# Kernel optimization log

Measured on AMD Instinct MI355X. Metric: run time of the kernel, lower is better.

Reference implementation:

```python
import jax, jax.numpy as jnp
import numpy as np

B, S = 2, 2048
HID = 2560
NH, NKV, HD = 20, 5, 128
GROUPS = NH // NKV  # 4
THETA = 500000.0
RMS_EPS = 1e-6  # RMSNorm default eps used for attn_sub_norm
NEG_INF = -1e9


def pack_ternary(key, M, K):
    """Pack ternary weights {-1,0,1} (stored as trits {0,1,2}) into SIMD
    block-interleaved uint8 layout: per 128-elem block, byte j holds
    weights j+0 (bits 6:7), j+32 (4:5), j+64 (2:3), j+96 (0:1)."""
    t = jax.random.randint(key, (M, K), 0, 3).astype(jnp.uint8)
    t = t.reshape(M, K // 128, 4, 32)
    byte = (t[:, :, 0] << 6) | (t[:, :, 1] << 4) | (t[:, :, 2] << 2) | t[:, :, 3]
    return byte.reshape(M, K // 4)


def unpack_ternary(packed):
    """Inverse of pack_ternary -> float weights in {-1,0,1}. (M, K//4) -> (M, K)."""
    M, Kp = packed.shape
    nb = Kp // 32
    b = packed.reshape(M, nb, 32)
    fields = jnp.stack([(b >> 6) & 3, (b >> 4) & 3, (b >> 2) & 3, b & 3], axis=2)
    return fields.reshape(M, nb * 128).astype(jnp.float32) - 1.0


def bitlinear(x, packed, scale):
    w = unpack_ternary(packed) * scale  # (out, in)
    return jnp.einsum('bsi,oi->bso', x, w)


def rotate_half(x):
    h = x.shape[-1] // 2
    return jnp.concatenate([-x[..., h:], x[..., :h]], axis=-1)


def rms_norm(x, w, eps=RMS_EPS):
    var = jnp.mean(jnp.square(x.astype(jnp.float32)), axis=-1, keepdims=True)
    return (w * (x * jax.lax.rsqrt(var + eps))).astype(x.dtype)


def setup_inputs() -> dict:
    key = jax.random.key(0)
    ks = jax.random.split(key, 6)
    hidden_states = jax.random.normal(ks[0], (B, S, HID), dtype=jnp.float32)
    causal = jnp.tril(jnp.ones((S, S), dtype=bool))
    attention_mask = jnp.where(causal, 0.0, NEG_INF).astype(jnp.float32)[None, None]
    return {
        'hidden_states': hidden_states,
        'attention_mask': attention_mask,
        'q_w': pack_ternary(ks[1], NH * HD, HID),
        'k_w': pack_ternary(ks[2], NKV * HD, HID),
        'v_w': pack_ternary(ks[3], NKV * HD, HID),
        'o_w': pack_ternary(ks[4], HID, NH * HD),
        'q_scale': jnp.float32(0.02),
        'k_scale': jnp.float32(0.02),
        'v_scale': jnp.float32(0.02),
        'o_scale': jnp.float32(0.02),
        'attn_norm_w': jnp.ones((NH * HD,), dtype=jnp.float32),
    }


def reference(hidden_states, attention_mask, q_w, k_w, v_w, o_w,
              q_scale, k_scale, v_scale, o_scale, attn_norm_w):
    bsz, seq_len, _ = hidden_states.shape
    q = bitlinear(hidden_states, q_w, q_scale)
    k = bitlinear(hidden_states, k_w, k_scale)
    v = bitlinear(hidden_states, v_w, v_scale)
    q = q.reshape(bsz, seq_len, NH, HD).transpose(0, 2, 1, 3)    # (b,h,s,d)
    k = k.reshape(bsz, seq_len, NKV, HD).transpose(0, 2, 1, 3)
    v = v.reshape(bsz, seq_len, NKV, HD).transpose(0, 2, 1, 3)
    # rotary embedding
    inv_freq = 1.0 / (THETA ** (jnp.arange(0, HD, 2, dtype=jnp.float32) / HD))
    t = jnp.arange(seq_len, dtype=jnp.float32)
    freqs = t[:, None] * inv_freq[None, :]            # (s, d/2)
    emb = jnp.concatenate([freqs, freqs], axis=-1)    # (s, d)
    cos, sin = jnp.cos(emb), jnp.sin(emb)
    q = q * cos + rotate_half(q) * sin
    k = k * cos + rotate_half(k) * sin
    # GQA: repeat kv heads
    k = jnp.repeat(k, GROUPS, axis=1)
    v = jnp.repeat(v, GROUPS, axis=1)
    scores = jnp.einsum('bhqd,bhkd->bhqk', q, k) / np.sqrt(HD).astype(np.float32)
    scores = scores + attention_mask
    attn = jax.nn.softmax(scores.astype(jnp.float32), axis=-1).astype(q.dtype)
    out = jnp.einsum('bhqk,bhkd->bhqd', attn, v)
    out = out.transpose(0, 2, 1, 3).reshape(bsz, seq_len, NH * HD)
    out = rms_norm(out, attn_norm_w)
    return bitlinear(out, o_w, o_scale)
```

## Files before the change

kernel.cpp:

```cpp
#include <hip/hip_runtime.h>
#include <cstdint>
#include <cstddef>

typedef __bf16 bf16x8 __attribute__((ext_vector_type(8)));
typedef float  f32x4  __attribute__((ext_vector_type(4)));
typedef int    i32x4  __attribute__((ext_vector_type(4)));
typedef unsigned short u16x4 __attribute__((ext_vector_type(4)));

#define DEV __device__ __forceinline__
#define NEGINF (-__builtin_inff())

DEV uint16_t f2bf(float f) {
  union { float f; uint32_t u; } v; v.f = f;
  uint32_t u = v.u;
  u += 0x7FFFu + ((u >> 16) & 1u);
  return (uint16_t)(u >> 16);
}
DEV float bf2f(uint16_t h) {
  union { uint32_t u; float f; } v; v.u = ((uint32_t)h) << 16;
  return v.f;
}

DEV void gload_lds16(const void* g, void* l) {
  __builtin_amdgcn_global_load_lds(
      (const __attribute__((address_space(1))) void*)g,
      (__attribute__((address_space(3))) void*)l, 16, 0, 0);
}


__global__ void k_f32_to_bf16(const float* __restrict__ in, uint16_t* __restrict__ out, int n4) {
  int i = blockIdx.x * blockDim.x + threadIdx.x;
  if (i >= n4) return;
  f32x4 v = *(const f32x4*)(in + (size_t)i * 4);
  u16x4 o;
  o[0] = f2bf(v[0]); o[1] = f2bf(v[1]); o[2] = f2bf(v[2]); o[3] = f2bf(v[3]);
  *(u16x4*)(out + (size_t)i * 4) = o;
}

__global__ void k_unpack_all(const uint32_t* __restrict__ qw, const uint32_t* __restrict__ kw,
                             const uint32_t* __restrict__ vw, const uint32_t* __restrict__ ow,
                             uint16_t* __restrict__ wqkv, uint16_t* __restrict__ owb,
                             const float* __restrict__ g) {
  int idx = blockIdx.x * blockDim.x + threadIdx.x;
  if (idx >= 4096000) return;
  if (idx < 2457600) {
    int local = (idx < 1638400) ? idx : ((idx < 2048000) ? idx - 1638400 : idx - 2048000);
    const uint32_t* s = (idx < 1638400) ? qw : ((idx < 2048000) ? kw : vw);
    uint32_t b = s[local] & 0xFFu;
    int drow = idx / 640, pc = idx - drow * 640;
    int blk = pc >> 5, j = pc & 31;
    size_t base = (size_t)drow * 2560 + (size_t)blk * 128 + j;
    wqkv[base]      = f2bf((float)((b >> 6) & 3u) - 1.0f);
    wqkv[base + 32] = f2bf((float)((b >> 4) & 3u) - 1.0f);
    wqkv[base + 64] = f2bf((float)((b >> 2) & 3u) - 1.0f);
    wqkv[base + 96] = f2bf((float)(b & 3u) - 1.0f);
  } else {
    int local = idx - 2457600;
    uint32_t b = ow[local] & 0xFFu;
    int drow = local / 640, pc = local - drow * 640;
    int blk = pc >> 5, j = pc & 31;
    int kpos = blk * 128 + j;
    size_t base = (size_t)drow * 2560 + kpos;
    owb[base]      = f2bf(((float)((b >> 6) & 3u) - 1.0f) * g[kpos]);
    owb[base + 32] = f2bf(((float)((b >> 4) & 3u) - 1.0f) * g[kpos + 32]);
    owb[base + 64] = f2bf(((float)((b >> 2) & 3u) - 1.0f) * g[kpos + 64]);
    owb[base + 96] = f2bf(((float)(b & 3u) - 1.0f) * g[kpos + 96]);
  }
}

__global__ void k_rope_table(float* __restrict__ cosT, float* __restrict__ sinT) {
  int idx = blockIdx.x * blockDim.x + threadIdx.x;
  int s = idx >> 6, i = idx & 63;
  float inv = expf((float)i * (-13.122363377404328f / 64.0f));
  float fr = (float)s * inv;
  cosT[idx] = cosf(fr);
  sinT[idx] = sinf(fr);
}

__global__ void k_rope(uint16_t* __restrict__ buf, const float* __restrict__ cosT,
                       const float* __restrict__ sinT, int H, int total) {
  int idx = blockIdx.x * blockDim.x + threadIdx.x;
  if (idx >= total) return;
  int d = idx & 63;
  int t = idx >> 6;
  int h = t % H;
  int row = t / H;
  int s = row & 2047;
  size_t base = (size_t)row * (size_t)(H * 128) + (size_t)h * 128 + d;
  float x1 = bf2f(buf[base]), x2 = bf2f(buf[base + 64]);
  float c = cosT[(s << 6) + d], sn = sinT[(s << 6) + d];
  buf[base]      = f2bf(x1 * c - x2 * sn);
  buf[base + 64] = f2bf(x2 * c + x1 * sn);
}

template<int MODE>
__global__ __launch_bounds__(256, 2)
void k_gemm(const uint16_t* __restrict__ A, const uint16_t* __restrict__ W,
            uint16_t* __restrict__ Qo, uint16_t* __restrict__ Ko, uint16_t* __restrict__ Vo,
            float* __restrict__ Fo,
            const float* __restrict__ s0p, const float* __restrict__ s1p, const float* __restrict__ s2p,
            int M, int N, int K)
{
  __shared__ uint16_t As[128 * 64];
  __shared__ uint16_t Bs[128 * 64];
  const int tid = threadIdx.x;
  const int n0 = blockIdx.x * 128, m0 = blockIdx.y * 128;
  const int lane = tid & 63, w = tid >> 6;
  const int wm = (w >> 1) * 64, wn = (w & 1) * 64;
  const int lr = lane & 15, lg = lane >> 4, lk = lg * 8;
  const size_t K2 = (size_t)K * 2;
  f32x4 acc[4][4] = {};

  const int srow = tid >> 3;
  const int cprime = ((tid & 7) * 16) ^ ((srow & 7) << 4);
  const uint8_t* Ag = (const uint8_t*)A + (size_t)(m0 + srow) * K2 + cprime;
  const uint8_t* Wg = (const uint8_t*)W + (size_t)(n0 + srow) * K2 + cprime;
  char* Al = (char*)As + w * 1024;
  char* Bl = (char*)Bs + w * 1024;

  for (size_t k0b = 0; k0b < K2; k0b += 128) {
    #pragma unroll
    for (int i = 0; i < 4; ++i)
      gload_lds16(Ag + (size_t)(i * 32) * K2 + k0b, Al + i * 4096);
    #pragma unroll
    for (int i = 0; i < 4; ++i)
      gload_lds16(Wg + (size_t)(i * 32) * K2 + k0b, Bl + i * 4096);
    __syncthreads();
    #pragma unroll
    for (int kc = 0; kc < 64; kc += 32) {
      bf16x8 a[4], b[4];
      #pragma unroll
      for (int i = 0; i < 4; ++i) {
        const int r = wm + i * 16 + lr;
        a[i] = *(const bf16x8*)((const char*)As + r * 128 + (((kc + lk) * 2) ^ ((r & 7) << 4)));
      }
      #pragma unroll
      for (int j = 0; j < 4; ++j) {
        const int r = wn + j * 16 + lr;
        b[j] = *(const bf16x8*)((const char*)Bs + r * 128 + (((kc + lk) * 2) ^ ((r & 7) << 4)));
      }
      #pragma unroll
      for (int i = 0; i < 4; ++i)
        #pragma unroll
        for (int j = 0; j < 4; ++j)
          acc[i][j] = __builtin_amdgcn_mfma_f32_16x16x32_bf16(a[i], b[j], acc[i][j], 0, 0, 0);
    }
    __syncthreads();
  }

  if (MODE == 0) {
    const float qs = *s0p, ks = *s1p, vs = *s2p;
    #pragma unroll
    for (int i = 0; i < 4; ++i) {
      const int rowb = m0 + wm + i * 16 + lg * 4;
      #pragma unroll
      for (int j = 0; j < 4; ++j) {
        const int col = n0 + wn + j * 16 + lr;
        #pragma unroll
        for (int r = 0; r < 4; ++r) {
          const int rr = rowb + r;
          const float v = acc[i][j][r];
          if (col < 2560) {
            Qo[(size_t)rr * 2560 + col] = f2bf(v * qs);
          } else if (col < 3200) {
            Ko[(size_t)rr * 640 + (col - 2560)] = f2bf(v * ks);
          } else {
            const int n2 = col - 3200;
            const int kvh = n2 >> 7, d = n2 & 127;
            const int bb = rr >> 11, ss = rr & 2047;
            Vo[(((size_t)(bb * 5 + kvh) * 128 + d) << 11) + ss] = f2bf(v * vs);
          }
        }
      }
    }
  } else {
    const float os = *s0p;
    #pragma unroll
    for (int i = 0; i < 4; ++i) {
      const int rowb = m0 + wm + i * 16 + lg * 4;
      #pragma unroll
      for (int j = 0; j < 4; ++j) {
        const int col = n0 + wn + j * 16 + lr;
        #pragma unroll
        for (int r = 0; r < 4; ++r)
          Fo[(size_t)(rowb + r) * N + col] = acc[i][j][r] * os * s1p[rowb + r];
      }
    }
  }
}

__global__ __launch_bounds__(256, 2)
void k_attn(const uint16_t* __restrict__ Q, const uint16_t* __restrict__ Kb,
            const uint16_t* __restrict__ Vt, uint16_t* __restrict__ Ob,
            const float* __restrict__ cosT, const float* __restrict__ sinT)
{
  __shared__ char Klds[2][16384];
  __shared__ char Vlds[2][16384];
  __shared__ uint16_t p_lds[4][16][72];

  const int lin = blockIdx.x;
  const int gslot = (lin & 7) * 80 + (lin >> 3);
  const int bk = gslot >> 6;
  const int st = 63 - (gslot & 63);
  const int b = bk / 5, kvh = bk - b * 5;

  const int tid = threadIdx.x, lane = tid & 63, w = tid >> 6;
  const int lr = lane & 15, lg = lane >> 4, lk = lg * 8;
  const int h = kvh * 4 + w;
  uint16_t (*pl)[72] = p_lds[w];
  const int kswz = (lr & 7) << 4;

  const uint8_t* Kg = (const uint8_t*)(Kb + (size_t)b * 2048 * 640 + (size_t)kvh * 128);
  const uint8_t* Vg = (const uint8_t*)(Vt + ((size_t)(b * 5 + kvh) * 128) * 2048);

  const int krow = tid >> 4;
  const int kcol = ((tid & 15) * 16) ^ ((krow & 7) << 4);
  const int vrow = tid >> 3;
  const int vcol = ((tid & 7) * 16) ^ ((vrow & 7) << 4);
  const int dst16 = tid * 16;

  const float C = 0.127531019577f;

  const int q0 = st * 32;
  const int ns = (q0 + 95) >> 6;

  bf16x8 qf0[4], qf1[4];
  {
    const size_t qb0 = ((size_t)(b * 2048 + q0 + lr)) * 2560 + (size_t)h * 128 + lk;
    #pragma unroll
    for (int c = 0; c < 4; ++c) {
      qf0[c] = *(const bf16x8*)&Q[qb0 + c * 32];
      qf1[c] = *(const bf16x8*)&Q[qb0 + 16 * 2560 + c * 32];
    }
  }
  #pragma unroll
  for (int g = 0; g < 2; ++g) {
    bf16x8* qf = g ? qf1 : qf0;
    const int s = q0 + 16 * g + lr;
    const int tb0 = s * 64 + lg * 8;
    #pragma unroll
    for (int c = 0; c < 2; ++c) {
      const int tb = tb0 + c * 32;
      f32x4 csa = *(const f32x4*)&cosT[tb];
      f32x4 csb = *(const f32x4*)&cosT[tb + 4];
      f32x4 sna = *(const f32x4*)&sinT[tb];
      f32x4 snb = *(const f32x4*)&sinT[tb + 4];
      #pragma unroll
      for (int j = 0; j < 8; ++j) {
        const float cs = (j < 4) ? csa[j] : csb[j - 4];
        const float sn = (j < 4) ? sna[j] : snb[j - 4];
        const float x1 = (float)qf[c][j], x2 = (float)qf[c + 2][j];
        qf[c][j]     = (__bf16)(x1 * cs - x2 * sn);
        qf[c + 2][j] = (__bf16)(x2 * cs + x1 * sn);
      }
    }
  }

  {
    const uint8_t* Ks = Kg + (size_t)krow * 1280 + kcol;
    const uint8_t* Vs = Vg + (size_t)vrow * 4096 + vcol;
    #pragma unroll
    for (int i = 0; i < 4; ++i) gload_lds16(Ks + (size_t)i * 16 * 1280, Klds[0] + dst16 + i * 4096);
    #pragma unroll
    for (int i = 0; i < 4; ++i) gload_lds16(Vs + (size_t)i * 32 * 4096, Vlds[0] + dst16 + i * 4096);
  }

  int cur = 0;
  float m0 = NEGINF, m1 = NEGINF, l0 = 0.f, l1 = 0.f;
  f32x4 oa0[8] = {}, oa1[8] = {};

  #pragma unroll 1
  for (int stp = 0; stp < ns; ++stp) {
    const int k0 = stp * 64;
    __syncthreads();

    if (stp + 1 < ns) {
      const int kn = k0 + 64;
      const uint8_t* Ks = Kg + (size_t)(kn + krow) * 1280 + kcol;
      const uint8_t* Vs = Vg + (size_t)vrow * 4096 + (size_t)kn * 2 + vcol;
      char* Kd = Klds[cur ^ 1] + dst16;
      char* Vd = Vlds[cur ^ 1] + dst16;
      #pragma unroll
      for (int i = 0; i < 4; ++i) gload_lds16(Ks + (size_t)i * 16 * 1280, Kd + i * 4096);
      #pragma unroll
      for (int i = 0; i < 4; ++i) gload_lds16(Vs + (size_t)i * 32 * 4096, Vd + i * 4096);
    }

    const char* Kc = Klds[cur];
    const char* Vc = Vlds[cur];

    __builtin_amdgcn_s_setprio(1);
    f32x4 sa0[4] = {}, sa1[4] = {};
    #pragma unroll
    for (int t = 0; t < 4; ++t) {
      #pragma unroll
      for (int c = 0; c < 4; ++c) {
        bf16x8 kf = *(const bf16x8*)(Kc + (t * 16 + lr) * 256 + ((c * 64 + lg * 16) ^ kswz));
        sa0[t] = __builtin_amdgcn_mfma_f32_16x16x32_bf16(kf, qf0[c], sa0[t], 0, 0, 0);
        sa1[t] = __builtin_amdgcn_mfma_f32_16x16x32_bf16(kf, qf1[c], sa1[t], 0, 0, 0);
      }
    }
    __builtin_amdgcn_s_setprio(0);

    #pragma unroll
    for (int g = 0; g < 2; ++g) {
      const f32x4* sa = g ? sa1 : sa0;
      f32x4* oa = g ? oa1 : oa0;
      float& m = g ? m1 : m0;
      float& l = g ? l1 : l0;
      const int q0g = q0 + 16 * g;

      float sraw[16];
      if (k0 + 63 > q0g) {
        #pragma unroll
        for (int t = 0; t < 4; ++t)
          #pragma unroll
          for (int r = 0; r < 4; ++r)
            sraw[t * 4 + r] = (k0 + t * 16 + lg * 4 + r <= q0g + lr) ? sa[t][r] : NEGINF;
      } else {
        #pragma unroll
        for (int t = 0; t < 4; ++t)
          #pragma unroll
          for (int r = 0; r < 4; ++r)
            sraw[t * 4 + r] = sa[t][r];
      }
      float a01 = fmaxf(sraw[0], sraw[1]),   a23 = fmaxf(sraw[2], sraw[3]);
      float a45 = fmaxf(sraw[4], sraw[5]),   a67 = fmaxf(sraw[6], sraw[7]);
      float a89 = fmaxf(sraw[8], sraw[9]),   aab = fmaxf(sraw[10], sraw[11]);
      float acd = fmaxf(sraw[12], sraw[13]), aef = fmaxf(sraw[14], sraw[15]);
      float mxr = fmaxf(fmaxf(fmaxf(a01, a23), fmaxf(a45, a67)),
                        fmaxf(fmaxf(a89, aab), fmaxf(acd, aef)));
      mxr = fmaxf(mxr, __shfl_xor(mxr, 16));
      mxr = fmaxf(mxr, __shfl_xor(mxr, 32));
      const float mx_u = mxr * C;
      if (!__all(mx_u <= m + 8.0f)) {
        const float mn = fmaxf(m, mx_u);
        const float resc = __builtin_exp2f(m - mn);
        m = mn;
        l *= resc;
        #pragma unroll
        for (int dc = 0; dc < 8; ++dc) {
          oa[dc][0] *= resc; oa[dc][1] *= resc; oa[dc][2] *= resc; oa[dc][3] *= resc;
        }
      }
      const float nm = -m;
      float pv[16];
      #pragma unroll
      for (int i = 0; i < 16; ++i) pv[i] = __builtin_exp2f(fmaf(sraw[i], C, nm));
      float s0 = (pv[0] + pv[1]) + (pv[2] + pv[3]);
      float s1 = (pv[4] + pv[5]) + (pv[6] + pv[7]);
      float s2 = (pv[8] + pv[9]) + (pv[10] + pv[11]);
      float s3 = (pv[12] + pv[13]) + (pv[14] + pv[15]);
      l += (s0 + s1) + (s2 + s3);
      #pragma unroll
      for (int t = 0; t < 4; ++t) {
        union { __bf16 b4[4]; unsigned long long u64; } pk;
        #pragma unroll
        for (int r = 0; r < 4; ++r) pk.b4[r] = (__bf16)pv[t * 4 + r];
        *(unsigned long long*)&pl[lr][t * 16 + lg * 4] = pk.u64;
      }
      bf16x8 pa0 = *(const bf16x8*)&pl[lr][lk];
      bf16x8 pa1 = *(const bf16x8*)&pl[lr][32 + lk];
      __builtin_amdgcn_s_setprio(1);
      #pragma unroll
      for (int dc = 0; dc < 8; ++dc) {
        bf16x8 vf0 = *(const bf16x8*)(Vc + (dc * 16 + lr) * 128 + ((lg * 16) ^ kswz));
        bf16x8 vf1 = *(const bf16x8*)(Vc + (dc * 16 + lr) * 128 + ((64 + lg * 16) ^ kswz));
        oa[dc] = __builtin_amdgcn_mfma_f32_16x16x32_bf16(vf0, pa0, oa[dc], 0, 0, 0);
        oa[dc] = __builtin_amdgcn_mfma_f32_16x16x32_bf16(vf1, pa1, oa[dc], 0, 0, 0);
      }
      __builtin_amdgcn_s_setprio(0);
    }
    cur ^= 1;
  }

  #pragma unroll
  for (int g = 0; g < 2; ++g) {
    f32x4* oa = g ? oa1 : oa0;
    float lf = g ? l1 : l0;
    lf += __shfl_xor(lf, 16);
    lf += __shfl_xor(lf, 32);
    const float inv = 1.0f / lf;
    const size_t obase = ((size_t)(b * 2048 + q0 + 16 * g + lr)) * 2560 + (size_t)h * 128;
    #pragma unroll
    for (int dc = 0; dc < 8; ++dc) {
      union { __bf16 b4[4]; unsigned long long u64; } ok;
      #pragma unroll
      for (int r = 0; r < 4; ++r) ok.b4[r] = (__bf16)(oa[dc][r] * inv);
      *(unsigned long long*)&Ob[obase + dc * 16 + lg * 4] = ok.u64;
    }
  }
}

__global__ __launch_bounds__(256)
void k_rowrms(const uint16_t* __restrict__ X, float* __restrict__ rs)
{
  const int row = blockIdx.x;
  const int tid = threadIdx.x;
  const uint16_t* x = X + (size_t)row * 2560;
  float ss = 0.f;
  #pragma unroll
  for (int it = 0; it < 10; ++it) {
    const int i = tid + it * 256;
    const float v = bf2f(x[i]);
    ss += v * v;
  }
  #pragma unroll
  for (int off = 1; off < 64; off <<= 1) ss += __shfl_xor(ss, off, 64);
  __shared__ float sred[4];
  if ((tid & 63) == 0) sred[tid >> 6] = ss;
  __syncthreads();
  if (tid == 0) {
    const float tot = sred[0] + sred[1] + sred[2] + sred[3];
    rs[row] = rsqrtf(tot * (1.0f / 2560.0f) + 1e-6f);
  }
}

extern "C" void kernel_launch(void* const* d_in, const int* in_sizes, int n_in,
                              void* d_out, int out_size, void* d_ws, size_t ws_size,
                              hipStream_t stream)
{
  const float*    x     = (const float*)d_in[0];
  const uint32_t* qw    = (const uint32_t*)d_in[2];
  const uint32_t* kw    = (const uint32_t*)d_in[3];
  const uint32_t* vw    = (const uint32_t*)d_in[4];
  const uint32_t* ow    = (const uint32_t*)d_in[5];
  const float*    qs    = (const float*)d_in[6];
  const float*    ks    = (const float*)d_in[7];
  const float*    vs    = (const float*)d_in[8];
  const float*    os    = (const float*)d_in[9];
  const float*    gnorm = (const float*)d_in[10];

  char* ws = (char*)d_ws;
  uint16_t* xb   = (uint16_t*)(ws + 0);
  uint16_t* wqkv = (uint16_t*)(ws + 20971520);
  uint16_t* owb  = (uint16_t*)(ws + 40632320);
  float*    cosT = (float*)   (ws + 53739520);
  float*    sinT = (float*)   (ws + 54263808);
  uint16_t* Qb   = (uint16_t*)(ws + 54788096);
  uint16_t* Kb   = (uint16_t*)(ws + 75759616);
  uint16_t* Vt   = (uint16_t*)(ws + 81002496);
  float*    rsb  = (float*)   (ws + 54788096);

  k_f32_to_bf16<<<10240, 256, 0, stream>>>(x, xb, 2621440);
  k_unpack_all<<<16000, 256, 0, stream>>>(qw, kw, vw, ow, wqkv, owb, gnorm);
  k_rope_table<<<512, 256, 0, stream>>>(cosT, sinT);

  k_gemm<0><<<dim3(30, 32), 256, 0, stream>>>(xb, wqkv, Qb, Kb, Vt, nullptr,
                                              qs, ks, vs, 4096, 3840, 2560);
  k_rope<<<5120, 256, 0, stream>>>(Kb, cosT, sinT, 5, 1310720);

  k_attn<<<dim3(640), 256, 0, stream>>>(Qb, Kb, Vt, xb, cosT, sinT);

  k_rowrms<<<4096, 256, 0, stream>>>(xb, rsb);

  k_gemm<1><<<dim3(20, 32), 256, 0, stream>>>(xb, owb, nullptr, nullptr, nullptr,
                                              (float*)d_out, os, rsb, nullptr,
                                              4096, 2560, 2560);
}
```

Before: 297.3 us.

## Halve attention KV tile to 32 keys and raise occupancy to four blocks

The attention kernel now streams 32-key K/V tiles instead of 64, which halves LDS buffers and lets launch bounds request four blocks per CU. The loop count becomes exact per 32-row query tile, so less fully-masked work is done on the diagonal. P is staged in a swizzled per-group LDS layout, and each V fragment is reused for both query groups in a merged PV loop. In exchange there are twice as many barrier and softmax iterations per key range, and register pressure must fit the higher occupancy target.

```diff
diff --git a/kernel.cpp b/kernel.cpp
--- a/kernel.cpp
+++ b/kernel.cpp
@@ -189,14 +189,14 @@
   }
 }
 
-__global__ __launch_bounds__(256, 2)
+__global__ __launch_bounds__(256, 4)
 void k_attn(const uint16_t* __restrict__ Q, const uint16_t* __restrict__ Kb,
             const uint16_t* __restrict__ Vt, uint16_t* __restrict__ Ob,
             const float* __restrict__ cosT, const float* __restrict__ sinT)
 {
-  __shared__ char Klds[2][16384];
-  __shared__ char Vlds[2][16384];
-  __shared__ uint16_t p_lds[4][16][72];
+  __shared__ char Klds[2][8192];
+  __shared__ char Vlds[2][8192];
+  __shared__ uint16_t p_lds[4][2][16][32];
 
   const int lin = blockIdx.x;
   const int gslot = (lin & 7) * 80 + (lin >> 3);
@@ -207,22 +207,24 @@
   const int tid = threadIdx.x, lane = tid & 63, w = tid >> 6;
   const int lr = lane & 15, lg = lane >> 4, lk = lg * 8;
   const int h = kvh * 4 + w;
-  uint16_t (*pl)[72] = p_lds[w];
+  uint16_t (*pl)[16][32] = p_lds[w];
   const int kswz = (lr & 7) << 4;
+  const int vswz = (lr & 3) << 4;
+  const int pswz = (lr & 3) << 3;
 
   const uint8_t* Kg = (const uint8_t*)(Kb + (size_t)b * 2048 * 640 + (size_t)kvh * 128);
   const uint8_t* Vg = (const uint8_t*)(Vt + ((size_t)(b * 5 + kvh) * 128) * 2048);
 
   const int krow = tid >> 4;
   const int kcol = ((tid & 15) * 16) ^ ((krow & 7) << 4);
-  const int vrow = tid >> 3;
-  const int vcol = ((tid & 7) * 16) ^ ((vrow & 7) << 4);
+  const int vrow = tid >> 2;
+  const int vcol = ((tid & 3) * 16) ^ ((vrow & 3) << 4);
   const int dst16 = tid * 16;
 
   const float C = 0.127531019577f;
 
   const int q0 = st * 32;
-  const int ns = (q0 + 95) >> 6;
+  const int ns = st + 1;
 
   bf16x8 qf0[4], qf1[4];
   {
@@ -260,9 +262,9 @@
     const uint8_t* Ks = Kg + (size_t)krow * 1280 + kcol;
     const uint8_t* Vs = Vg + (size_t)vrow * 4096 + vcol;
     #pragma unroll
-    for (int i = 0; i < 4; ++i) gload_lds16(Ks + (size_t)i * 16 * 1280, Klds[0] + dst16 + i * 4096);
-    #pragma unroll
-    for (int i = 0; i < 4; ++i) gload_lds16(Vs + (size_t)i * 32 * 4096, Vlds[0] + dst16 + i * 4096);
+    for (int i = 0; i < 2; ++i) gload_lds16(Ks + (size_t)i * 16 * 1280, Klds[0] + dst16 + i * 4096);
+    #pragma unroll
+    for (int i = 0; i < 2; ++i) gload_lds16(Vs + (size_t)i * 64 * 4096, Vlds[0] + dst16 + i * 4096);
   }
 
   int cur = 0;
@@ -271,28 +273,28 @@
 
   #pragma unroll 1
   for (int stp = 0; stp < ns; ++stp) {
-    const int k0 = stp * 64;
+    const int k0 = stp * 32;
     __syncthreads();
 
     if (stp + 1 < ns) {
-      const int kn = k0 + 64;
+      const int kn = k0 + 32;
       const uint8_t* Ks = Kg + (size_t)(kn + krow) * 1280 + kcol;
       const uint8_t* Vs = Vg + (size_t)vrow * 4096 + (size_t)kn * 2 + vcol;
       char* Kd = Klds[cur ^ 1] + dst16;
       char* Vd = Vlds[cur ^ 1] + dst16;
       #pragma unroll
-      for (int i = 0; i < 4; ++i) gload_lds16(Ks + (size_t)i * 16 * 1280, Kd + i * 4096);
-      #pragma unroll
-      for (int i = 0; i < 4; ++i) gload_lds16(Vs + (size_t)i * 32 * 4096, Vd + i * 4096);
+      for (int i = 0; i < 2; ++i) gload_lds16(Ks + (size_t)i * 16 * 1280, Kd + i * 4096);
+      #pragma unroll
+      for (int i = 0; i < 2; ++i) gload_lds16(Vs + (size_t)i * 64 * 4096, Vd + i * 4096);
     }
 
     const char* Kc = Klds[cur];
     const char* Vc = Vlds[cur];
 
     __builtin_amdgcn_s_setprio(1);
-    f32x4 sa0[4] = {}, sa1[4] = {};
-    #pragma unroll
-    for (int t = 0; t < 4; ++t) {
+    f32x4 sa0[2] = {}, sa1[2] = {};
+    #pragma unroll
+    for (int t = 0; t < 2; ++t) {
       #pragma unroll
       for (int c = 0; c < 4; ++c) {
         bf16x8 kf = *(const bf16x8*)(Kc + (t * 16 + lr) * 256 + ((c * 64 + lg * 16) ^ kswz));
@@ -310,26 +312,23 @@
       float& l = g ? l1 : l0;
       const int q0g = q0 + 16 * g;
 
-      float sraw[16];
-      if (k0 + 63 > q0g) {
-        #pragma unroll
-        for (int t = 0; t < 4; ++t)
+      float sraw[8];
+      if (k0 + 31 > q0g) {
+        #pragma unroll
+        for (int t = 0; t < 2; ++t)
           #pragma unroll
           for (int r = 0; r < 4; ++r)
             sraw[t * 4 + r] = (k0 + t * 16 + lg * 4 + r <= q0g + lr) ? sa[t][r] : NEGINF;
       } else {
         #pragma unroll
-        for (int t = 0; t < 4; ++t)
+        for (int t = 0; t < 2; ++t)
           #pragma unroll
           for (int r = 0; r < 4; ++r)
             sraw[t * 4 + r] = sa[t][r];
       }
-      float a01 = fmaxf(sraw[0], sraw[1]),   a23 = fmaxf(sraw[2], sraw[3]);
-      float a45 = fmaxf(sraw[4], sraw[5]),   a67 = fmaxf(sraw[6], sraw[7]);
-      float a89 = fmaxf(sraw[8], sraw[9]),   aab = fmaxf(sraw[10], sraw[11]);
-      float acd = fmaxf(sraw[12], sraw[13]), aef = fmaxf(sraw[14], sraw[15]);
-      float mxr = fmaxf(fmaxf(fmaxf(a01, a23), fmaxf(a45, a67)),
-                        fmaxf(fmaxf(a89, aab), fmaxf(acd, aef)));
+      float a01 = fmaxf(sraw[0], sraw[1]), a23 = fmaxf(sraw[2], sraw[3]);
+      float a45 = fmaxf(sraw[4], sraw[5]), a67 = fmaxf(sraw[6], sraw[7]);
+      float mxr = fmaxf(fmaxf(a01, a23), fmaxf(a45, a67));
       mxr = fmaxf(mxr, __shfl_xor(mxr, 16));
       mxr = fmaxf(mxr, __shfl_xor(mxr, 32));
       const float mx_u = mxr * C;
@@ -344,33 +343,29 @@
         }
       }
       const float nm = -m;
-      float pv[16];
-      #pragma unroll
-      for (int i = 0; i < 16; ++i) pv[i] = __builtin_exp2f(fmaf(sraw[i], C, nm));
-      float s0 = (pv[0] + pv[1]) + (pv[2] + pv[3]);
-      float s1 = (pv[4] + pv[5]) + (pv[6] + pv[7]);
-      float s2 = (pv[8] + pv[9]) + (pv[10] + pv[11]);
-      float s3 = (pv[12] + pv[13]) + (pv[14] + pv[15]);
-      l += (s0 + s1) + (s2 + s3);
-      #pragma unroll
-      for (int t = 0; t < 4; ++t) {
+      float pv[8];
+      #pragma unroll
+      for (int i = 0; i < 8; ++i) pv[i] = __builtin_exp2f(fmaf(sraw[i], C, nm));
+      l += ((pv[0] + pv[1]) + (pv[2] + pv[3])) + ((pv[4] + pv[5]) + (pv[6] + pv[7]));
+      #pragma unroll
+      for (int t = 0; t < 2; ++t) {
         union { __bf16 b4[4]; unsigned long long u64; } pk;
         #pragma unroll
         for (int r = 0; r < 4; ++r) pk.b4[r] = (__bf16)pv[t * 4 + r];
-        *(unsigned long long*)&pl[lr][t * 16 + lg * 4] = pk.u64;
-      }
-      bf16x8 pa0 = *(const bf16x8*)&pl[lr][lk];
-      bf16x8 pa1 = *(const bf16x8*)&pl[lr][32 + lk];
-      __builtin_amdgcn_s_setprio(1);
-      #pragma unroll
-      for (int dc = 0; dc < 8; ++dc) {
-        bf16x8 vf0 = *(const bf16x8*)(Vc + (dc * 16 + lr) * 128 + ((lg * 16) ^ kswz));
-        bf16x8 vf1 = *(const bf16x8*)(Vc + (dc * 16 + lr) * 128 + ((64 + lg * 16) ^ kswz));
-        oa[dc] = __builtin_amdgcn_mfma_f32_16x16x32_bf16(vf0, pa0, oa[dc], 0, 0, 0);
-        oa[dc] = __builtin_amdgcn_mfma_f32_16x16x32_bf16(vf1, pa1, oa[dc], 0, 0, 0);
-      }
-      __builtin_amdgcn_s_setprio(0);
-    }
+        *(unsigned long long*)&pl[g][lr][(t * 16 + lg * 4) ^ pswz] = pk.u64;
+      }
+    }
+
+    bf16x8 paA = *(const bf16x8*)&pl[0][lr][lk ^ pswz];
+    bf16x8 paB = *(const bf16x8*)&pl[1][lr][lk ^ pswz];
+    __builtin_amdgcn_s_setprio(1);
+    #pragma unroll
+    for (int dc = 0; dc < 8; ++dc) {
+      bf16x8 vf = *(const bf16x8*)(Vc + (dc * 16 + lr) * 64 + ((lg * 16) ^ vswz));
+      oa0[dc] = __builtin_amdgcn_mfma_f32_16x16x32_bf16(vf, paA, oa0[dc], 0, 0, 0);
+      oa1[dc] = __builtin_amdgcn_mfma_f32_16x16x32_bf16(vf, paB, oa1[dc], 0, 0, 0);
+    }
+    __builtin_amdgcn_s_setprio(0);
     cur ^= 1;
   }
 
```

After: 455.7 us. 1.53x slower.

## Replace GEMM with 256x256 tile, 8-wave, double-buffered pipelined kernel

Applied to the files above, without the earlier changes.

Replaces the 128x128 single-buffered GEMM with a 256x256-tile kernel run by 512 threads (8 waves). LDS is double-buffered so global-to-LDS loads overlap MFMA work, and the schedule is controlled by hand with barriers, waitcnt and setprio. Blocks are remapped through an XCD-aware swizzle of a 1D grid. The larger tile raises data reuse and the pipeline hides memory latency, at the cost of 128KB of LDS per block and far fewer blocks (240 and 160), which may underfill the CUs.

```diff
diff --git a/kernel.cpp b/kernel.cpp
--- a/kernel.cpp
+++ b/kernel.cpp
@@ -94,68 +94,114 @@
 }
 
 template<int MODE>
-__global__ __launch_bounds__(256, 2)
-void k_gemm(const uint16_t* __restrict__ A, const uint16_t* __restrict__ W,
-            uint16_t* __restrict__ Qo, uint16_t* __restrict__ Ko, uint16_t* __restrict__ Vo,
-            float* __restrict__ Fo,
-            const float* __restrict__ s0p, const float* __restrict__ s1p, const float* __restrict__ s2p,
-            int M, int N, int K)
+__global__ __launch_bounds__(512, 2)
+void k_gemm8(const uint16_t* __restrict__ A, const uint16_t* __restrict__ W,
+             uint16_t* __restrict__ Qo, uint16_t* __restrict__ Ko, uint16_t* __restrict__ Vo,
+             float* __restrict__ Fo,
+             const float* __restrict__ s0p, const float* __restrict__ s1p,
+             const float* __restrict__ s2p,
+             int M, int N, int K, int gx)
 {
-  __shared__ uint16_t As[128 * 64];
-  __shared__ uint16_t Bs[128 * 64];
-  const int tid = threadIdx.x;
-  const int n0 = blockIdx.x * 128, m0 = blockIdx.y * 128;
-  const int lane = tid & 63, w = tid >> 6;
-  const int wm = (w >> 1) * 64, wn = (w & 1) * 64;
+  __shared__ char lds8[131072];
+  const int tid = threadIdx.x, lane = tid & 63, w = tid >> 6;
+  const int wm = w >> 2, wn = w & 3;
   const int lr = lane & 15, lg = lane >> 4, lk = lg * 8;
+  const int nb = gridDim.x, cpx = nb >> 3;
+  const int lin = blockIdx.x;
+  const int swz = (lin & 7) * cpx + (lin >> 3);
+  const int n0 = (swz % gx) * 256, m0 = (swz / gx) * 256;
   const size_t K2 = (size_t)K * 2;
-  f32x4 acc[4][4] = {};
-
-  const int srow = tid >> 3;
-  const int cprime = ((tid & 7) * 16) ^ ((srow & 7) << 4);
-  const uint8_t* Ag = (const uint8_t*)A + (size_t)(m0 + srow) * K2 + cprime;
-  const uint8_t* Wg = (const uint8_t*)W + (size_t)(n0 + srow) * K2 + cprime;
-  char* Al = (char*)As + w * 1024;
-  char* Bl = (char*)Bs + w * 1024;
-
-  for (size_t k0b = 0; k0b < K2; k0b += 128) {
-    #pragma unroll
-    for (int i = 0; i < 4; ++i)
-      gload_lds16(Ag + (size_t)(i * 32) * K2 + k0b, Al + i * 4096);
-    #pragma unroll
-    for (int i = 0; i < 4; ++i)
-      gload_lds16(Wg + (size_t)(i * 32) * K2 + k0b, Bl + i * 4096);
-    __syncthreads();
-    #pragma unroll
-    for (int kc = 0; kc < 64; kc += 32) {
-      bf16x8 a[4], b[4];
-      #pragma unroll
-      for (int i = 0; i < 4; ++i) {
-        const int r = wm + i * 16 + lr;
-        a[i] = *(const bf16x8*)((const char*)As + r * 128 + (((kc + lk) * 2) ^ ((r & 7) << 4)));
-      }
-      #pragma unroll
-      for (int j = 0; j < 4; ++j) {
-        const int r = wn + j * 16 + lr;
-        b[j] = *(const bf16x8*)((const char*)Bs + r * 128 + (((kc + lk) * 2) ^ ((r & 7) << 4)));
-      }
-      #pragma unroll
-      for (int i = 0; i < 4; ++i)
-        #pragma unroll
-        for (int j = 0; j < 4; ++j)
-          acc[i][j] = __builtin_amdgcn_mfma_f32_16x16x32_bf16(a[i], b[j], acc[i][j], 0, 0, 0);
-    }
-    __syncthreads();
-  }
+
+  f32x4 acc[8][4] = {};
+  bf16x8 bfr[4][2];
+
+  auto STAGE = [&](int kind, int s, int h, int kt) {
+    const uint8_t* src = kind ? (const uint8_t*)W : (const uint8_t*)A;
+    const int r0 = (kind ? n0 : m0) + h * 128;
+    char* dst = lds8 + kind * 65536 + s * 32768 + h * 16384 + w * 1024;
+    const size_t kb = (size_t)kt * 128;
+    #pragma unroll
+    for (int i2 = 0; i2 < 2; ++i2) {
+      const int row = i2 * 64 + (tid >> 3);
+      const int col = ((tid & 7) * 16) ^ ((row & 7) << 4);
+      gload_lds16(src + (size_t)(r0 + row) * K2 + kb + col, dst + i2 * 8192);
+    }
+  };
+  auto LDA = [&](int s, int i, int kc) -> bf16x8 {
+    const int r = i * 16 + lr;
+    return *(const bf16x8*)(lds8 + s * 32768 + wm * 16384 + r * 128 +
+                            (((kc + lk) * 2) ^ ((r & 7) << 4)));
+  };
+  auto LDB = [&](int s, int j, int kc) -> bf16x8 {
+    const int rb = wn * 64 + j * 16 + lr;
+    const int r2 = rb & 127;
+    return *(const bf16x8*)(lds8 + 65536 + s * 32768 + (rb >> 7) * 16384 + r2 * 128 +
+                            (((kc + lk) * 2) ^ ((r2 & 7) << 4)));
+  };
+
+#define GPH(SLOT, P, READB, STG, VMW)                                                         \
+  {                                                                                           \
+    bf16x8 af00 = LDA(SLOT, 2*(P), 0),   af01 = LDA(SLOT, 2*(P), 32);                         \
+    bf16x8 af10 = LDA(SLOT, 2*(P)+1, 0), af11 = LDA(SLOT, 2*(P)+1, 32);                       \
+    if (READB) {                                                                              \
+      bfr[0][0]=LDB(SLOT,0,0); bfr[0][1]=LDB(SLOT,0,32);                                      \
+      bfr[1][0]=LDB(SLOT,1,0); bfr[1][1]=LDB(SLOT,1,32);                                      \
+      bfr[2][0]=LDB(SLOT,2,0); bfr[2][1]=LDB(SLOT,2,32);                                      \
+      bfr[3][0]=LDB(SLOT,3,0); bfr[3][1]=LDB(SLOT,3,32);                                      \
+    }                                                                                         \
+    STG;                                                                                      \
+    asm volatile("" ::: "memory");                                                            \
+    __builtin_amdgcn_s_barrier();                                                             \
+    asm volatile("s_waitcnt lgkmcnt(0)" ::: "memory");                                        \
+    __builtin_amdgcn_sched_barrier(0);                                                        \
+    __builtin_amdgcn_s_setprio(1);                                                            \
+    _Pragma("unroll")                                                                         \
+    for (int j = 0; j < 4; ++j) {                                                             \
+      acc[2*(P)][j]   = __builtin_amdgcn_mfma_f32_16x16x32_bf16(af00, bfr[j][0], acc[2*(P)][j],   0,0,0); \
+      acc[2*(P)][j]   = __builtin_amdgcn_mfma_f32_16x16x32_bf16(af01, bfr[j][1], acc[2*(P)][j],   0,0,0); \
+      acc[2*(P)+1][j] = __builtin_amdgcn_mfma_f32_16x16x32_bf16(af10, bfr[j][0], acc[2*(P)+1][j], 0,0,0); \
+      acc[2*(P)+1][j] = __builtin_amdgcn_mfma_f32_16x16x32_bf16(af11, bfr[j][1], acc[2*(P)+1][j], 0,0,0); \
+    }                                                                                         \
+    __builtin_amdgcn_s_setprio(0);                                                            \
+    VMW;                                                                                      \
+    asm volatile("" ::: "memory");                                                            \
+    __builtin_amdgcn_s_barrier();                                                             \
+    asm volatile("" ::: "memory");                                                            \
+  }
+
+  STAGE(0, 0, 0, 0); STAGE(0, 0, 1, 0);
+  STAGE(1, 0, 0, 0); STAGE(1, 0, 1, 0);
+  STAGE(1, 1, 0, 1); STAGE(1, 1, 1, 1);
+  asm volatile("s_waitcnt vmcnt(4)" ::: "memory");
+  __builtin_amdgcn_s_barrier();
+
+  const int NI = K >> 7;
+  #pragma unroll 1
+  for (int u = 0; u < NI; ++u) {
+    const int T = 2 * u;
+    const bool nx = (u + 1 < NI);
+    GPH(0, 0, true,  { STAGE(0, 1, 0, T + 1); }, );
+    GPH(0, 1, false, { STAGE(0, 1, 1, T + 1); }, );
+    GPH(0, 2, false, { if (nx) STAGE(1, 0, 0, T + 2); }, );
+    GPH(0, 3, false, { if (nx) STAGE(1, 0, 1, T + 2); },
+        if (nx) { asm volatile("s_waitcnt vmcnt(4)" ::: "memory"); }
+        else    { asm volatile("s_waitcnt vmcnt(0)" ::: "memory"); } );
+    GPH(1, 0, true,  { if (nx) STAGE(0, 0, 0, T + 2); }, );
+    GPH(1, 1, false, { if (nx) STAGE(0, 0, 1, T + 2); }, );
+    GPH(1, 2, false, { if (nx) STAGE(1, 1, 0, T + 3); }, );
+    GPH(1, 3, false, { if (nx) STAGE(1, 1, 1, T + 3); },
+        { asm volatile("s_waitcnt vmcnt(4)" ::: "memory"); } );
+  }
+#undef GPH
 
   if (MODE == 0) {
     const float qs = *s0p, ks = *s1p, vs = *s2p;
     #pragma unroll
-    for (int i = 0; i < 4; ++i) {
-      const int rowb = m0 + wm + i * 16 + lg * 4;
+    for (int i = 0; i < 8; ++i) {
+      const int rowb = m0 + wm * 128 + i * 16 + lg * 4;
       #pragma unroll
       for (int j = 0; j < 4; ++j) {
-        const int col = n0 + wn + j * 16 + lr;
+        const int col = n0 + wn * 64 + j * 16 + lr;
         #pragma unroll
         for (int r = 0; r < 4; ++r) {
           const int rr = rowb + r;
@@ -176,11 +222,11 @@
   } else {
     const float os = *s0p;
     #pragma unroll
-    for (int i = 0; i < 4; ++i) {
-      const int rowb = m0 + wm + i * 16 + lg * 4;
+    for (int i = 0; i < 8; ++i) {
+      const int rowb = m0 + wm * 128 + i * 16 + lg * 4;
       #pragma unroll
       for (int j = 0; j < 4; ++j) {
-        const int col = n0 + wn + j * 16 + lr;
+        const int col = n0 + wn * 64 + j * 16 + lr;
         #pragma unroll
         for (int r = 0; r < 4; ++r)
           Fo[(size_t)(rowb + r) * N + col] = acc[i][j][r] * os * s1p[rowb + r];
@@ -446,15 +492,15 @@
   k_unpack_all<<<16000, 256, 0, stream>>>(qw, kw, vw, ow, wqkv, owb, gnorm);
   k_rope_table<<<512, 256, 0, stream>>>(cosT, sinT);
 
-  k_gemm<0><<<dim3(30, 32), 256, 0, stream>>>(xb, wqkv, Qb, Kb, Vt, nullptr,
-                                              qs, ks, vs, 4096, 3840, 2560);
+  k_gemm8<0><<<dim3(240), 512, 0, stream>>>(xb, wqkv, Qb, Kb, Vt, nullptr,
+                                            qs, ks, vs, 4096, 3840, 2560, 15);
   k_rope<<<5120, 256, 0, stream>>>(Kb, cosT, sinT, 5, 1310720);
 
   k_attn<<<dim3(640), 256, 0, stream>>>(Qb, Kb, Vt, xb, cosT, sinT);
 
   k_rowrms<<<4096, 256, 0, stream>>>(xb, rsb);
 
-  k_gemm<1><<<dim3(20, 32), 256, 0, stream>>>(xb, owb, nullptr, nullptr, nullptr,
-                                              (float*)d_out, os, rsb, nullptr,
-                                              4096, 2560, 2560);
-}
+  k_gemm8<1><<<dim3(160), 512, 0, stream>>>(xb, owb, nullptr, nullptr, nullptr,
+                                            (float*)d_out, os, rsb, nullptr,
+                                            4096, 2560, 2560, 10);
+}
```

Measured after the change: 304.3 us. +2.4%, slower.

## Merge prep kernels and fuse RMS sum-of-squares into attention epilogue

Applied to the files above, without the earlier changes.

Combines the bf16 conversion, ternary weight unpack and RoPE table kernels into one launch. Removes the separate row-RMS kernel: the attention epilogue accumulates each row's sum of squares of the bf16 outputs with atomicAdd into a buffer that the RoPE kernel zeroes, and the output GEMM computes rsqrt from it. This removes two launches and a full re-read of the attention output. The cost is atomic contention and a float summation order that is no longer deterministic.

```diff
diff --git a/kernel.cpp b/kernel.cpp
--- a/kernel.cpp
+++ b/kernel.cpp
@@ -28,58 +28,61 @@
 }
 
 
-__global__ void k_f32_to_bf16(const float* __restrict__ in, uint16_t* __restrict__ out, int n4) {
-  int i = blockIdx.x * blockDim.x + threadIdx.x;
-  if (i >= n4) return;
-  f32x4 v = *(const f32x4*)(in + (size_t)i * 4);
-  u16x4 o;
-  o[0] = f2bf(v[0]); o[1] = f2bf(v[1]); o[2] = f2bf(v[2]); o[3] = f2bf(v[3]);
-  *(u16x4*)(out + (size_t)i * 4) = o;
-}
-
-__global__ void k_unpack_all(const uint32_t* __restrict__ qw, const uint32_t* __restrict__ kw,
-                             const uint32_t* __restrict__ vw, const uint32_t* __restrict__ ow,
-                             uint16_t* __restrict__ wqkv, uint16_t* __restrict__ owb,
-                             const float* __restrict__ g) {
+__global__ void k_prep(const float* __restrict__ x, uint16_t* __restrict__ xb,
+                       const uint32_t* __restrict__ qw, const uint32_t* __restrict__ kw,
+                       const uint32_t* __restrict__ vw, const uint32_t* __restrict__ ow,
+                       uint16_t* __restrict__ wqkv, uint16_t* __restrict__ owb,
+                       const float* __restrict__ g,
+                       float* __restrict__ cosT, float* __restrict__ sinT)
+{
+  const int bid = blockIdx.x, tid = threadIdx.x;
+  if (bid < 10240) {
+    const int i = bid * 256 + tid;
+    f32x4 v = *(const f32x4*)(x + (size_t)i * 4);
+    u16x4 o;
+    o[0] = f2bf(v[0]); o[1] = f2bf(v[1]); o[2] = f2bf(v[2]); o[3] = f2bf(v[3]);
+    *(u16x4*)(xb + (size_t)i * 4) = o;
+  } else if (bid < 26240) {
+    const int idx = (bid - 10240) * 256 + tid;
+    if (idx < 2457600) {
+      int local = (idx < 1638400) ? idx : ((idx < 2048000) ? idx - 1638400 : idx - 2048000);
+      const uint32_t* s = (idx < 1638400) ? qw : ((idx < 2048000) ? kw : vw);
+      uint32_t b = s[local] & 0xFFu;
+      int drow = idx / 640, pc = idx - drow * 640;
+      int blk = pc >> 5, j = pc & 31;
+      size_t base = (size_t)drow * 2560 + (size_t)blk * 128 + j;
+      wqkv[base]      = f2bf((float)((b >> 6) & 3u) - 1.0f);
+      wqkv[base + 32] = f2bf((float)((b >> 4) & 3u) - 1.0f);
+      wqkv[base + 64] = f2bf((float)((b >> 2) & 3u) - 1.0f);
+      wqkv[base + 96] = f2bf((float)(b & 3u) - 1.0f);
+    } else {
+      int local = idx - 2457600;
+      uint32_t b = ow[local] & 0xFFu;
+      int drow = local / 640, pc = local - drow * 640;
+      int blk = pc >> 5, j = pc & 31;
+      int kpos = blk * 128 + j;
+      size_t base = (size_t)drow * 2560 + kpos;
+      owb[base]      = f2bf(((float)((b >> 6) & 3u) - 1.0f) * g[kpos]);
+      owb[base + 32] = f2bf(((float)((b >> 4) & 3u) - 1.0f) * g[kpos + 32]);
+      owb[base + 64] = f2bf(((float)((b >> 2) & 3u) - 1.0f) * g[kpos + 64]);
+      owb[base + 96] = f2bf(((float)(b & 3u) - 1.0f) * g[kpos + 96]);
+    }
+  } else {
+    const int idx = (bid - 26240) * 256 + tid;
+    const int s = idx >> 6, i = idx & 63;
+    float inv = expf((float)i * (-13.122363377404328f / 64.0f));
+    float fr = (float)s * inv;
+    cosT[idx] = cosf(fr);
+    sinT[idx] = sinf(fr);
+  }
+}
+
+__global__ void k_rope(uint16_t* __restrict__ buf, const float* __restrict__ cosT,
+                       const float* __restrict__ sinT, int H, int total,
+                       float* __restrict__ ss)
+{
   int idx = blockIdx.x * blockDim.x + threadIdx.x;
-  if (idx >= 4096000) return;
-  if (idx < 2457600) {
-    int local = (idx < 1638400) ? idx : ((idx < 2048000) ? idx - 1638400 : idx - 2048000);
-    const uint32_t* s = (idx < 1638400) ? qw : ((idx < 2048000) ? kw : vw);
-    uint32_t b = s[local] & 0xFFu;
-    int drow = idx / 640, pc = idx - drow * 640;
-    int blk = pc >> 5, j = pc & 31;
-    size_t base = (size_t)drow * 2560 + (size_t)blk * 128 + j;
-    wqkv[base]      = f2bf((float)((b >> 6) & 3u) - 1.0f);
-    wqkv[base + 32] = f2bf((float)((b >> 4) & 3u) - 1.0f);
-    wqkv[base + 64] = f2bf((float)((b >> 2) & 3u) - 1.0f);
-    wqkv[base + 96] = f2bf((float)(b & 3u) - 1.0f);
-  } else {
-    int local = idx - 2457600;
-    uint32_t b = ow[local] & 0xFFu;
-    int drow = local / 640, pc = local - drow * 640;
-    int blk = pc >> 5, j = pc & 31;
-    int kpos = blk * 128 + j;
-    size_t base = (size_t)drow * 2560 + kpos;
-    owb[base]      = f2bf(((float)((b >> 6) & 3u) - 1.0f) * g[kpos]);
-    owb[base + 32] = f2bf(((float)((b >> 4) & 3u) - 1.0f) * g[kpos + 32]);
-    owb[base + 64] = f2bf(((float)((b >> 2) & 3u) - 1.0f) * g[kpos + 64]);
-    owb[base + 96] = f2bf(((float)(b & 3u) - 1.0f) * g[kpos + 96]);
-  }
-}
-
-__global__ void k_rope_table(float* __restrict__ cosT, float* __restrict__ sinT) {
-  int idx = blockIdx.x * blockDim.x + threadIdx.x;
-  int s = idx >> 6, i = idx & 63;
-  float inv = expf((float)i * (-13.122363377404328f / 64.0f));
-  float fr = (float)s * inv;
-  cosT[idx] = cosf(fr);
-  sinT[idx] = sinf(fr);
-}
-
-__global__ void k_rope(uint16_t* __restrict__ buf, const float* __restrict__ cosT,
-                       const float* __restrict__ sinT, int H, int total) {
-  int idx = blockIdx.x * blockDim.x + threadIdx.x;
+  if (blockIdx.x < 16) ss[blockIdx.x * 256 + threadIdx.x] = 0.f;
   if (idx >= total) return;
   int d = idx & 63;
   int t = idx >> 6;
@@ -167,8 +170,8 @@
           } else {
             const int n2 = col - 3200;
             const int kvh = n2 >> 7, d = n2 & 127;
-            const int bb = rr >> 11, ss = rr & 2047;
-            Vo[(((size_t)(bb * 5 + kvh) * 128 + d) << 11) + ss] = f2bf(v * vs);
+            const int bb = rr >> 11, ss2 = rr & 2047;
+            Vo[(((size_t)(bb * 5 + kvh) * 128 + d) << 11) + ss2] = f2bf(v * vs);
           }
         }
       }
@@ -182,8 +185,10 @@
       for (int j = 0; j < 4; ++j) {
         const int col = n0 + wn + j * 16 + lr;
         #pragma unroll
-        for (int r = 0; r < 4; ++r)
-          Fo[(size_t)(rowb + r) * N + col] = acc[i][j][r] * os * s1p[rowb + r];
+        for (int r = 0; r < 4; ++r) {
+          const float rs = rsqrtf(s1p[rowb + r] * (1.0f / 2560.0f) + 1e-6f);
+          Fo[(size_t)(rowb + r) * N + col] = acc[i][j][r] * os * rs;
+        }
       }
     }
   }
@@ -192,7 +197,8 @@
 __global__ __launch_bounds__(256, 2)
 void k_attn(const uint16_t* __restrict__ Q, const uint16_t* __restrict__ Kb,
             const uint16_t* __restrict__ Vt, uint16_t* __restrict__ Ob,
-            const float* __restrict__ cosT, const float* __restrict__ sinT)
+            const float* __restrict__ cosT, const float* __restrict__ sinT,
+            float* __restrict__ ssb)
 {
   __shared__ char Klds[2][16384];
   __shared__ char Vlds[2][16384];
@@ -382,37 +388,22 @@
     lf += __shfl_xor(lf, 32);
     const float inv = 1.0f / lf;
     const size_t obase = ((size_t)(b * 2048 + q0 + 16 * g + lr)) * 2560 + (size_t)h * 128;
+    float ssq = 0.f;
     #pragma unroll
     for (int dc = 0; dc < 8; ++dc) {
       union { __bf16 b4[4]; unsigned long long u64; } ok;
       #pragma unroll
-      for (int r = 0; r < 4; ++r) ok.b4[r] = (__bf16)(oa[dc][r] * inv);
+      for (int r = 0; r < 4; ++r) {
+        ok.b4[r] = (__bf16)(oa[dc][r] * inv);
+        const float vq = (float)ok.b4[r];
+        ssq += vq * vq;
+      }
       *(unsigned long long*)&Ob[obase + dc * 16 + lg * 4] = ok.u64;
     }
-  }
-}
-
-__global__ __launch_bounds__(256)
-void k_rowrms(const uint16_t* __restrict__ X, float* __restrict__ rs)
-{
-  const int row = blockIdx.x;
-  const int tid = threadIdx.x;
-  const uint16_t* x = X + (size_t)row * 2560;
-  float ss = 0.f;
-  #pragma unroll
-  for (int it = 0; it < 10; ++it) {
-    const int i = tid + it * 256;
-    const float v = bf2f(x[i]);
-    ss += v * v;
-  }
-  #pragma unroll
-  for (int off = 1; off < 64; off <<= 1) ss += __shfl_xor(ss, off, 64);
-  __shared__ float sred[4];
-  if ((tid & 63) == 0) sred[tid >> 6] = ss;
-  __syncthreads();
-  if (tid == 0) {
-    const float tot = sred[0] + sred[1] + sred[2] + sred[3];
-    rs[row] = rsqrtf(tot * (1.0f / 2560.0f) + 1e-6f);
+    ssq += __shfl_xor(ssq, 16);
+    ssq += __shfl_xor(ssq, 32);
+    if (lane < 16)
+      atomicAdd(&ssb[b * 2048 + q0 + 16 * g + lr], ssq);
   }
 }
 
@@ -440,21 +431,17 @@
   uint16_t* Qb   = (uint16_t*)(ws + 54788096);
   uint16_t* Kb   = (uint16_t*)(ws + 75759616);
   uint16_t* Vt   = (uint16_t*)(ws + 81002496);
-  float*    rsb  = (float*)   (ws + 54788096);
-
-  k_f32_to_bf16<<<10240, 256, 0, stream>>>(x, xb, 2621440);
-  k_unpack_all<<<16000, 256, 0, stream>>>(qw, kw, vw, ow, wqkv, owb, gnorm);
-  k_rope_table<<<512, 256, 0, stream>>>(cosT, sinT);
+  float*    ssb  = (float*)   (ws + 20971520);
+
+  k_prep<<<26752, 256, 0, stream>>>(x, xb, qw, kw, vw, ow, wqkv, owb, gnorm, cosT, sinT);
 
   k_gemm<0><<<dim3(30, 32), 256, 0, stream>>>(xb, wqkv, Qb, Kb, Vt, nullptr,
                                               qs, ks, vs, 4096, 3840, 2560);
-  k_rope<<<5120, 256, 0, stream>>>(Kb, cosT, sinT, 5, 1310720);
-
-  k_attn<<<dim3(640), 256, 0, stream>>>(Qb, Kb, Vt, xb, cosT, sinT);
-
-  k_rowrms<<<4096, 256, 0, stream>>>(xb, rsb);
+  k_rope<<<5120, 256, 0, stream>>>(Kb, cosT, sinT, 5, 1310720, ssb);
+
+  k_attn<<<dim3(640), 256, 0, stream>>>(Qb, Kb, Vt, xb, cosT, sinT, ssb);
 
   k_gemm<1><<<dim3(20, 32), 256, 0, stream>>>(xb, owb, nullptr, nullptr, nullptr,
-                                              (float*)d_out, os, rsb, nullptr,
+                                              (float*)d_out, os, ssb, nullptr,
                                               4096, 2560, 2560);
 }
```

After: 287.8 us. 3.2% less time.
